# Kernel optimization log

Hardware: AMD Instinct MI355X
Metric: run time of the kernel (lower is better)

Reference implementation:

```python
import jax, jax.numpy as jnp
import numpy as np

B, T, N, D = 16, 64, 22, 64
K, E, DT, H = 4, 8, 5, 64
KL_WEIGHT = 0.01


def setup_inputs() -> dict:
    key = jax.random.key(0)
    ks = jax.random.split(key, 4)
    x = jax.random.normal(ks[0], (B, T, N, D), jnp.float32)
    # fixed-degree neighbor table: joint j's neighbors are (j..j+3) mod N, self first
    nb = jnp.asarray((np.arange(N)[:, None] + np.arange(K)[None, :]) % N, jnp.int32)
    Fin = DT * K * D  # 1280 flattened local window feature
    W1 = jax.random.normal(ks[1], (N, E, Fin, H), jnp.float32) / np.float32(np.sqrt(Fin))
    b1 = jnp.zeros((N, E, H), jnp.float32)
    W2 = jax.random.normal(ks[2], (N, E, H, H), jnp.float32) / np.float32(np.sqrt(H))
    b2 = jnp.zeros((N, E, H), jnp.float32)
    W3 = jax.random.normal(ks[3], (N, E, H, D), jnp.float32) / np.float32(np.sqrt(H))
    b3 = jnp.zeros((N, E, D), jnp.float32)
    return {"x": x, "nb": nb, "W1": W1, "b1": b1, "W2": W2, "b2": b2, "W3": W3, "b3": b3}


def reference(x, nb, W1, b1, W2, b2, W3, b3):
    Bx, Tx, Nx, Dx = x.shape
    dt_half = DT // 2
    # all valid centers t in range(dt_half, T - dt_half - 1), batched (no python loop over t, j)
    ts = jnp.arange(dt_half, Tx - dt_half - 1)            # [Tw]
    offs = jnp.arange(-dt_half, dt_half + 1)              # [DT]
    win = x[:, ts[:, None] + offs[None, :]]               # [B,Tw,DT,N,D]
    dx = win[:, :, :, nb, :]                              # [B,Tw,DT,N,K,D] neighbor gather
    Tw = ts.shape[0]
    f = dx.transpose(0, 1, 3, 2, 4, 5).reshape(Bx, Tw, Nx, DT * K * Dx)  # [B,Tw,N,Fin]
    # per-joint per-expert MLP, fully batched
    h = jax.nn.relu(jnp.einsum('btnf,nefh->btneh', f, W1) + b1)
    h = jax.nn.relu(jnp.einsum('btneh,nehg->btneg', h, W2) + b2)
    pred = jnp.einsum('btneh,nehd->btned', h, W3) + b3    # [B,Tw,N,E,D]
    y = x[:, ts]                                          # [B,Tw,N,D] center-frame target
    err = jnp.mean((pred - y[:, :, :, None, :]) ** 2, axis=-1)  # [B,Tw,N,E]
    min_err = jnp.min(err, axis=-1)                       # winner-take-all (monopoly)
    expert_idx_all = jnp.argmin(err, axis=-1)             # [B,Tw,N]
    p = jax.nn.softmax(-err, axis=-1)
    kl = jnp.sum(p * (jnp.log(p + 1e-9) + jnp.log(jnp.float32(E))), axis=-1)  # KL to uniform
    per_tj = jnp.mean(min_err + KL_WEIGHT * kl, axis=0)   # [Tw,N] batch-mean local losses
    # original divides by the FINAL loop indices j and t (off-by-one kept for fidelity)
    total = jnp.sum(per_tj) / jnp.float32(Nx - 1) / jnp.float32(Tx - dt_half - 2)
    expert_idx = expert_idx_all[:, -1, -1]                # last (t, j) iteration, [B]
    return total, expert_idx
```

## Files before the change

kernel.cpp:

```cpp
#include <hip/hip_runtime.h>
#include <math.h>

#define B_   16
#define T_   64
#define N_   22
#define D_   64
#define K_   4
#define E_   8
#define H_   64
#define TW   59
#define M_   (B_ * TW)
#define NE_  (N_ * E_)
#define NDXT (N_ * D_)
#define XTOT (B_ * T_ * N_ * D_)

typedef __attribute__((ext_vector_type(8))) short short8;
typedef __attribute__((ext_vector_type(4))) float float4v;

union Frag {
    short8 s8;
    unsigned u[4];
};

#define ERRWS_BYTES  ((size_t)(M_ * N_ * E_) * 4)
#define XH_OFF       (ERRWS_BYTES)
#define XIMG_BYTES   ((size_t)XTOT * 2)
#define XL_OFF       (XH_OFF + XIMG_BYTES)

#define HIMG_ROW 68

__device__ inline void split2(float f, unsigned& hi, unsigned& lo) {
    unsigned u  = __float_as_uint(f);
    unsigned ht = u & 0xffff0000u;
    float rem   = f - __uint_as_float(ht);
    hi = u >> 16;
    lo = __float_as_uint(rem) >> 16;
}

__global__ __launch_bounds__(256) void xsplit_kernel(
    const float* __restrict__ x, short* __restrict__ xh, short* __restrict__ xl)
{
    int i = (blockIdx.x * 256 + threadIdx.x) * 4;
    if (i >= XTOT) return;
    float4 v = *(const float4*)(x + i);
    unsigned h0, h1, h2, h3, l0, l1, l2, l3;
    split2(v.x, h0, l0); split2(v.y, h1, l1);
    split2(v.z, h2, l2); split2(v.w, h3, l3);
    uint2 hp, lp;
    hp.x = h0 | (h1 << 16); hp.y = h2 | (h3 << 16);
    lp.x = l0 | (l1 << 16); lp.y = l2 | (l3 << 16);
    *(uint2*)(xh + i) = hp;
    *(uint2*)(xl + i) = lp;
}

__global__ __launch_bounds__(256, 3) void moe_err_kernel(
    const float* __restrict__ x, const short* __restrict__ xh,
    const short* __restrict__ xl, const int* __restrict__ nb,
    const float* __restrict__ W1, const float* __restrict__ W2,
    const float* __restrict__ W3,
    const float* __restrict__ b1, const float* __restrict__ b2,
    const float* __restrict__ b3, float* __restrict__ err_ws)
{
    const int tid = threadIdx.x;
    const int w   = tid >> 6;
    const int L   = tid & 63;
    const int g   = blockIdx.x;
    const int e   = g & 7;
    const int mt  = (g >> 3) & 7;
    const int n   = g >> 6;
    const int ne  = n * E_ + e;

    __shared__ __align__(16) char smem[51200];
    unsigned char* wbuf = (unsigned char*)smem;
    unsigned* himg = (unsigned*)(smem + 16384);

    const int lrow = L & 15;
    const int dseg = (L >> 4) * 8;
    const int ccol = L & 15;
    const int qrow = (L >> 4) * 4;
    const int rowbase = mt * 128 + w * 32;

    const short* xhrow[2];
    const short* xlrow[2];
    #pragma unroll
    for (int rt = 0; rt < 2; ++rt) {
        int m  = rowbase + rt * 16 + lrow;
        int mc = m < M_ ? m : M_ - 1;
        int b = mc / TW, t = mc % TW;
        size_t base = (size_t)(b * T_ + t) * NDXT;
        xhrow[rt] = xh + base;
        xlrow[rt] = xl + base;
    }

    const int o0 = __builtin_amdgcn_readfirstlane(nb[n * K_ + 0]) * D_;
    const int o1 = __builtin_amdgcn_readfirstlane(nb[n * K_ + 1]) * D_;
    const int o2 = __builtin_amdgcn_readfirstlane(nb[n * K_ + 2]) * D_;
    const int o3 = __builtin_amdgcn_readfirstlane(nb[n * K_ + 3]) * D_;

    const float* W1ne = W1 + (size_t)ne * (1280 * 64);
    const float* W2ne = W2 + (size_t)ne * 4096;
    const float* W3ne = W3 + (size_t)ne * 4096;

    float wf[2][8];
    uint4 wph[2], wpl[2];
    auto loadWf = [&](const float* src) {
        #pragma unroll
        for (int p = 0; p < 2; ++p) {
            const int pi = 2 * w + p;
            const float* sp = src + ((pi >> 2) * 32 + (L >> 4) * 8) * 64
                                  + ((pi & 3) * 16 + (L & 15));
            #pragma unroll
            for (int j = 0; j < 8; ++j) wf[p][j] = sp[j * 64];
        }
    };
    auto packW = [&]() {
        #pragma unroll
        for (int p = 0; p < 2; ++p) {
            unsigned hs[8], ls[8];
            #pragma unroll
            for (int j = 0; j < 8; ++j) split2(wf[p][j], hs[j], ls[j]);
            wph[p].x = hs[0] | (hs[1] << 16); wph[p].y = hs[2] | (hs[3] << 16);
            wph[p].z = hs[4] | (hs[5] << 16); wph[p].w = hs[6] | (hs[7] << 16);
            wpl[p].x = ls[0] | (ls[1] << 16); wpl[p].y = ls[2] | (ls[3] << 16);
            wpl[p].z = ls[4] | (ls[5] << 16); wpl[p].w = ls[6] | (ls[7] << 16);
        }
    };
    auto storeW = [&]() {
        #pragma unroll
        for (int p = 0; p < 2; ++p) {
            char* bp = (char*)wbuf + (size_t)(2 * w + p) * 2048 + (size_t)L * 16;
            *(uint4*)bp          = wph[p];
            *(uint4*)(bp + 1024) = wpl[p];
        }
    };
    auto bfrag = [&](int s2, int cf, int hl) -> short8 {
        return *(const short8*)(wbuf + (size_t)((s2 * 4 + cf) * 2 + hl) * 1024
                                     + (size_t)L * 16);
    };

    loadWf(W1ne);
    packW();

    float4v acc1[2][4];
    #pragma unroll
    for (int rt = 0; rt < 2; ++rt)
        #pragma unroll
        for (int cf = 0; cf < 4; ++cf) acc1[rt][cf] = (float4v)0.f;

    for (int dt = 0; dt < 5; ++dt) {
        #pragma unroll
        for (int kk = 0; kk < 4; ++kk) {
            const int c = dt * 4 + kk;
            __syncthreads();
            storeW();
            __syncthreads();

            const float* nsrc = (c < 19) ? (W1ne + (size_t)(c + 1) * 4096) : W2ne;
            loadWf(nsrc);

            const int okk = (kk == 0) ? o0 : ((kk == 1) ? o1 : ((kk == 2) ? o2 : o3));
            const int off = dt * NDXT + okk;

            Frag ah[2][2], al[2][2];
            #pragma unroll
            for (int s2 = 0; s2 < 2; ++s2)
                #pragma unroll
                for (int rt = 0; rt < 2; ++rt) {
                    ah[s2][rt].s8 = *(const short8*)(xhrow[rt] + off + s2 * 32 + dseg);
                    al[s2][rt].s8 = *(const short8*)(xlrow[rt] + off + s2 * 32 + dseg);
                }
            #pragma unroll
            for (int s2 = 0; s2 < 2; ++s2)
                #pragma unroll
                for (int cf = 0; cf < 4; ++cf) {
                    short8 bh = bfrag(s2, cf, 0);
                    short8 bl = bfrag(s2, cf, 1);
                    #pragma unroll
                    for (int rt = 0; rt < 2; ++rt) {
                        acc1[rt][cf] = __builtin_amdgcn_mfma_f32_16x16x32_bf16(ah[s2][rt].s8, bh, acc1[rt][cf], 0, 0, 0);
                        acc1[rt][cf] = __builtin_amdgcn_mfma_f32_16x16x32_bf16(ah[s2][rt].s8, bl, acc1[rt][cf], 0, 0, 0);
                        acc1[rt][cf] = __builtin_amdgcn_mfma_f32_16x16x32_bf16(al[s2][rt].s8, bh, acc1[rt][cf], 0, 0, 0);
                    }
                }
            packW();
        }
    }

    __syncthreads();
    storeW();
    loadWf(W3ne);
    #pragma unroll
    for (int cf = 0; cf < 4; ++cf) {
        float bv = b1[(size_t)ne * H_ + cf * 16 + ccol];
        #pragma unroll
        for (int rt = 0; rt < 2; ++rt)
            #pragma unroll
            for (int reg = 0; reg < 4; ++reg) {
                float hv = fmaxf(acc1[rt][cf][reg] + bv, 0.f);
                unsigned u  = __float_as_uint(hv);
                unsigned ht = u & 0xffff0000u;
                float rem   = hv - __uint_as_float(ht);
                himg[(w * 32 + rt * 16 + qrow + reg) * HIMG_ROW + cf * 16 + ccol] =
                    ht | (__float_as_uint(rem) >> 16);
            }
    }
    packW();
    __syncthreads();

    float4v acc2[2][4];
    #pragma unroll
    for (int rt = 0; rt < 2; ++rt)
        #pragma unroll
        for (int cf = 0; cf < 4; ++cf) acc2[rt][cf] = (float4v)0.f;
    #pragma unroll
    for (int s2 = 0; s2 < 2; ++s2) {
        Frag ah[2], al[2];
        #pragma unroll
        for (int rt = 0; rt < 2; ++rt) {
            const unsigned* hp = himg + (w * 32 + rt * 16 + lrow) * HIMG_ROW + s2 * 32 + dseg;
            uint4 u0 = *(const uint4*)hp;
            uint4 u1 = *(const uint4*)(hp + 4);
            unsigned uu[8] = {u0.x, u0.y, u0.z, u0.w, u1.x, u1.y, u1.z, u1.w};
            #pragma unroll
            for (int i = 0; i < 4; ++i) {
                ah[rt].u[i] = (uu[2 * i] >> 16) | (uu[2 * i + 1] & 0xffff0000u);
                al[rt].u[i] = (uu[2 * i] & 0xffffu) | (uu[2 * i + 1] << 16);
            }
        }
        #pragma unroll
        for (int cf = 0; cf < 4; ++cf) {
            short8 bh = bfrag(s2, cf, 0);
            short8 bl = bfrag(s2, cf, 1);
            #pragma unroll
            for (int rt = 0; rt < 2; ++rt) {
                acc2[rt][cf] = __builtin_amdgcn_mfma_f32_16x16x32_bf16(ah[rt].s8, bh, acc2[rt][cf], 0, 0, 0);
                acc2[rt][cf] = __builtin_amdgcn_mfma_f32_16x16x32_bf16(ah[rt].s8, bl, acc2[rt][cf], 0, 0, 0);
                acc2[rt][cf] = __builtin_amdgcn_mfma_f32_16x16x32_bf16(al[rt].s8, bh, acc2[rt][cf], 0, 0, 0);
            }
        }
    }

    __syncthreads();
    storeW();
    #pragma unroll
    for (int cf = 0; cf < 4; ++cf) {
        float bv = b2[(size_t)ne * H_ + cf * 16 + ccol];
        #pragma unroll
        for (int rt = 0; rt < 2; ++rt)
            #pragma unroll
            for (int reg = 0; reg < 4; ++reg) {
                float hv = fmaxf(acc2[rt][cf][reg] + bv, 0.f);
                unsigned u  = __float_as_uint(hv);
                unsigned ht = u & 0xffff0000u;
                float rem   = hv - __uint_as_float(ht);
                himg[(w * 32 + rt * 16 + qrow + reg) * HIMG_ROW + cf * 16 + ccol] =
                    ht | (__float_as_uint(rem) >> 16);
            }
    }
    __syncthreads();

    float4v acc3[2][4];
    #pragma unroll
    for (int rt = 0; rt < 2; ++rt)
        #pragma unroll
        for (int cf = 0; cf < 4; ++cf) acc3[rt][cf] = (float4v)0.f;
    #pragma unroll
    for (int s2 = 0; s2 < 2; ++s2) {
        Frag ah[2], al[2];
        #pragma unroll
        for (int rt = 0; rt < 2; ++rt) {
            const unsigned* hp = himg + (w * 32 + rt * 16 + lrow) * HIMG_ROW + s2 * 32 + dseg;
            uint4 u0 = *(const uint4*)hp;
            uint4 u1 = *(const uint4*)(hp + 4);
            unsigned uu[8] = {u0.x, u0.y, u0.z, u0.w, u1.x, u1.y, u1.z, u1.w};
            #pragma unroll
            for (int i = 0; i < 4; ++i) {
                ah[rt].u[i] = (uu[2 * i] >> 16) | (uu[2 * i + 1] & 0xffff0000u);
                al[rt].u[i] = (uu[2 * i] & 0xffffu) | (uu[2 * i + 1] << 16);
            }
        }
        #pragma unroll
        for (int cf = 0; cf < 4; ++cf) {
            short8 bh = bfrag(s2, cf, 0);
            short8 bl = bfrag(s2, cf, 1);
            #pragma unroll
            for (int rt = 0; rt < 2; ++rt) {
                acc3[rt][cf] = __builtin_amdgcn_mfma_f32_16x16x32_bf16(ah[rt].s8, bh, acc3[rt][cf], 0, 0, 0);
                acc3[rt][cf] = __builtin_amdgcn_mfma_f32_16x16x32_bf16(ah[rt].s8, bl, acc3[rt][cf], 0, 0, 0);
                acc3[rt][cf] = __builtin_amdgcn_mfma_f32_16x16x32_bf16(al[rt].s8, bh, acc3[rt][cf], 0, 0, 0);
            }
        }
    }

    {
        float b3v[4];
        #pragma unroll
        for (int cf = 0; cf < 4; ++cf) b3v[cf] = b3[(size_t)ne * D_ + cf * 16 + ccol];

        #pragma unroll
        for (int rt = 0; rt < 2; ++rt) {
            #pragma unroll
            for (int reg = 0; reg < 4; ++reg) {
                const int m  = rowbase + rt * 16 + qrow + reg;
                const int mc = m < M_ ? m : M_ - 1;
                const int b = mc / TW, t = mc % TW;
                const float* yp = x + ((size_t)(b * T_ + t + 2) * N_ + n) * D_;
                float s = 0.f;
                #pragma unroll
                for (int cf = 0; cf < 4; ++cf) {
                    float d = acc3[rt][cf][reg] + b3v[cf] - yp[cf * 16 + ccol];
                    s += d * d;
                }
                s += __shfl_xor(s, 1);
                s += __shfl_xor(s, 2);
                s += __shfl_xor(s, 4);
                s += __shfl_xor(s, 8);
                if (ccol == 0 && m < M_) {
                    err_ws[((size_t)m * N_ + n) * E_ + e] = s * (1.f / 64.f);
                }
            }
        }
    }
}

__global__ __launch_bounds__(256) void moe_reduce_kernel(
    const float* __restrict__ err_ws, float* __restrict__ out)
{
    const int tid = threadIdx.x;
    const int idx = blockIdx.x * 256 + tid;
    float v = 0.f;
    if (idx < M_ * N_) {
        const int m = idx / N_, n = idx % N_;
        const float* ep = err_ws + (size_t)idx * E_;
        float ev[E_];
        float mn = ep[0];
        int am = 0;
        ev[0] = mn;
        #pragma unroll
        for (int i = 1; i < E_; ++i) {
            ev[i] = ep[i];
            if (ev[i] < mn) { mn = ev[i]; am = i; }
        }
        float p[E_];
        float Z = 0.f;
        #pragma unroll
        for (int i = 0; i < E_; ++i) { p[i] = expf(mn - ev[i]); Z += p[i]; }
        const float invZ = 1.f / Z;
        float kl = 0.f;
        #pragma unroll
        for (int i = 0; i < E_; ++i) {
            float q = p[i] * invZ;
            kl += q * (logf(q + 1e-9f) + 2.0794415416798357f);
        }
        v = mn + 0.01f * kl;
        const int t = m % TW, b = m / TW;
        if (t == TW - 1 && n == N_ - 1) out[1 + b] = (float)am;
    }
    __shared__ float sd[256];
    sd[tid] = v;
    __syncthreads();
    for (int s = 128; s > 0; s >>= 1) {
        if (tid < s) sd[tid] += sd[tid + s];
        __syncthreads();
    }
    if (tid == 0) atomicAdd(out, sd[0] * (1.f / 20160.f));
}

__global__ void init_out_kernel(float* out)
{
    if (threadIdx.x == 0) out[0] = 0.f;
}

extern "C" void kernel_launch(void* const* d_in, const int* in_sizes, int n_in,
                              void* d_out, int out_size, void* d_ws, size_t ws_size,
                              hipStream_t stream)
{
    const float* x  = (const float*)d_in[0];
    const int*   nb = (const int*)d_in[1];
    const float* W1 = (const float*)d_in[2];
    const float* b1 = (const float*)d_in[3];
    const float* W2 = (const float*)d_in[4];
    const float* b2 = (const float*)d_in[5];
    const float* W3 = (const float*)d_in[6];
    const float* b3 = (const float*)d_in[7];
    float* out    = (float*)d_out;
    float* err_ws = (float*)d_ws;
    short* xh     = (short*)((char*)d_ws + XH_OFF);
    short* xl     = (short*)((char*)d_ws + XL_OFF);

    hipLaunchKernelGGL(init_out_kernel, dim3(1), dim3(64), 0, stream, out);
    hipLaunchKernelGGL(xsplit_kernel, dim3(1408), dim3(256), 0, stream, x, xh, xl);
    hipLaunchKernelGGL(moe_err_kernel, dim3(NE_ * 8), dim3(256), 0, stream,
                       x, xh, xl, nb, W1, W2, W3, b1, b2, b3, err_ws);
    const int nred = (M_ * N_ + 255) / 256;
    hipLaunchKernelGGL(moe_reduce_kernel, dim3(nred), dim3(256), 0, stream, err_ws, out);
}
```

Before: 254.9 us.

## Double-buffer weight prefetch, reorder block mapping, single-block reduce without init kernel

Weight chunks for the first layer are now prefetched two stages ahead into a double-buffered register set, which hides global load latency behind the MFMA work. Blocks are remapped so consecutive block ids share the same expert and differ by row tile, which improves L2 reuse of the expert's weights. The reduction becomes one 1024-thread block that loops over all rows, uses vectorised loads and writes the total directly, so the init kernel and the atomic are no longer needed. In exchange the double buffer raises register pressure, which can hurt occupancy at 3 waves per SIMD, and the single-block reduce serialises that stage.

```diff
diff --git a/kernel.cpp b/kernel.cpp
--- a/kernel.cpp
+++ b/kernel.cpp
@@ -65,8 +65,8 @@
     const int w   = tid >> 6;
     const int L   = tid & 63;
     const int g   = blockIdx.x;
-    const int e   = g & 7;
-    const int mt  = (g >> 3) & 7;
+    const int mt  = g & 7;
+    const int e   = (g >> 3) & 7;
     const int n   = g >> 6;
     const int ne  = n * E_ + e;
 
@@ -100,25 +100,28 @@
     const float* W1ne = W1 + (size_t)ne * (1280 * 64);
     const float* W2ne = W2 + (size_t)ne * 4096;
     const float* W3ne = W3 + (size_t)ne * 4096;
-
-    float wf[2][8];
+    auto csrc = [&](int c) {
+        return c < 20 ? (W1ne + (size_t)c * 4096) : (c == 20 ? W2ne : W3ne);
+    };
+
+    float wf[2][2][8];
     uint4 wph[2], wpl[2];
-    auto loadWf = [&](const float* src) {
+    auto loadWf = [&](int wb, const float* src) {
         #pragma unroll
         for (int p = 0; p < 2; ++p) {
             const int pi = 2 * w + p;
             const float* sp = src + ((pi >> 2) * 32 + (L >> 4) * 8) * 64
                                   + ((pi & 3) * 16 + (L & 15));
             #pragma unroll
-            for (int j = 0; j < 8; ++j) wf[p][j] = sp[j * 64];
-        }
-    };
-    auto packW = [&]() {
+            for (int j = 0; j < 8; ++j) wf[wb][p][j] = sp[j * 64];
+        }
+    };
+    auto packW = [&](int wb) {
         #pragma unroll
         for (int p = 0; p < 2; ++p) {
             unsigned hs[8], ls[8];
             #pragma unroll
-            for (int j = 0; j < 8; ++j) split2(wf[p][j], hs[j], ls[j]);
+            for (int j = 0; j < 8; ++j) split2(wf[wb][p][j], hs[j], ls[j]);
             wph[p].x = hs[0] | (hs[1] << 16); wph[p].y = hs[2] | (hs[3] << 16);
             wph[p].z = hs[4] | (hs[5] << 16); wph[p].w = hs[6] | (hs[7] << 16);
             wpl[p].x = ls[0] | (ls[1] << 16); wpl[p].y = ls[2] | (ls[3] << 16);
@@ -138,8 +141,9 @@
                                      + (size_t)L * 16);
     };
 
-    loadWf(W1ne);
-    packW();
+    loadWf(0, csrc(0));
+    loadWf(1, csrc(1));
+    packW(0);
 
     float4v acc1[2][4];
     #pragma unroll
@@ -155,8 +159,7 @@
             storeW();
             __syncthreads();
 
-            const float* nsrc = (c < 19) ? (W1ne + (size_t)(c + 1) * 4096) : W2ne;
-            loadWf(nsrc);
+            loadWf(c & 1, csrc(c + 2 <= 21 ? c + 2 : 21));
 
             const int okk = (kk == 0) ? o0 : ((kk == 1) ? o1 : ((kk == 2) ? o2 : o3));
             const int off = dt * NDXT + okk;
@@ -182,13 +185,12 @@
                         acc1[rt][cf] = __builtin_amdgcn_mfma_f32_16x16x32_bf16(al[s2][rt].s8, bh, acc1[rt][cf], 0, 0, 0);
                     }
                 }
-            packW();
+            packW((c + 1) & 1);
         }
     }
 
     __syncthreads();
     storeW();
-    loadWf(W3ne);
     #pragma unroll
     for (int cf = 0; cf < 4; ++cf) {
         float bv = b1[(size_t)ne * H_ + cf * 16 + ccol];
@@ -204,7 +206,7 @@
                     ht | (__float_as_uint(rem) >> 16);
             }
     }
-    packW();
+    packW(1);
     __syncthreads();
 
     float4v acc2[2][4];
@@ -323,22 +325,23 @@
     }
 }
 
-__global__ __launch_bounds__(256) void moe_reduce_kernel(
+__global__ __launch_bounds__(1024) void moe_reduce_kernel(
     const float* __restrict__ err_ws, float* __restrict__ out)
 {
     const int tid = threadIdx.x;
-    const int idx = blockIdx.x * 256 + tid;
-    float v = 0.f;
-    if (idx < M_ * N_) {
+    float partial = 0.f;
+    for (int idx = tid; idx < M_ * N_; idx += 1024) {
         const int m = idx / N_, n = idx % N_;
         const float* ep = err_ws + (size_t)idx * E_;
         float ev[E_];
-        float mn = ep[0];
+        float4 e0 = *(const float4*)ep;
+        float4 e1 = *(const float4*)(ep + 4);
+        ev[0] = e0.x; ev[1] = e0.y; ev[2] = e0.z; ev[3] = e0.w;
+        ev[4] = e1.x; ev[5] = e1.y; ev[6] = e1.z; ev[7] = e1.w;
+        float mn = ev[0];
         int am = 0;
-        ev[0] = mn;
         #pragma unroll
         for (int i = 1; i < E_; ++i) {
-            ev[i] = ep[i];
             if (ev[i] < mn) { mn = ev[i]; am = i; }
         }
         float p[E_];
@@ -352,23 +355,18 @@
             float q = p[i] * invZ;
             kl += q * (logf(q + 1e-9f) + 2.0794415416798357f);
         }
-        v = mn + 0.01f * kl;
+        partial += mn + 0.01f * kl;
         const int t = m % TW, b = m / TW;
         if (t == TW - 1 && n == N_ - 1) out[1 + b] = (float)am;
     }
-    __shared__ float sd[256];
-    sd[tid] = v;
-    __syncthreads();
-    for (int s = 128; s > 0; s >>= 1) {
+    __shared__ float sd[1024];
+    sd[tid] = partial;
+    __syncthreads();
+    for (int s = 512; s > 0; s >>= 1) {
         if (tid < s) sd[tid] += sd[tid + s];
         __syncthreads();
     }
-    if (tid == 0) atomicAdd(out, sd[0] * (1.f / 20160.f));
-}
-
-__global__ void init_out_kernel(float* out)
-{
-    if (threadIdx.x == 0) out[0] = 0.f;
+    if (tid == 0) out[0] = sd[0] * (1.f / 20160.f);
 }
 
 extern "C" void kernel_launch(void* const* d_in, const int* in_sizes, int n_in,
@@ -388,10 +386,8 @@
     short* xh     = (short*)((char*)d_ws + XH_OFF);
     short* xl     = (short*)((char*)d_ws + XL_OFF);
 
-    hipLaunchKernelGGL(init_out_kernel, dim3(1), dim3(64), 0, stream, out);
     hipLaunchKernelGGL(xsplit_kernel, dim3(1408), dim3(256), 0, stream, x, xh, xl);
     hipLaunchKernelGGL(moe_err_kernel, dim3(NE_ * 8), dim3(256), 0, stream,
                        x, xh, xl, nb, W1, W2, W3, b1, b2, b3, err_ws);
-    const int nred = (M_ * N_ + 255) / 256;
-    hipLaunchKernelGGL(moe_reduce_kernel, dim3(nred), dim3(256), 0, stream, err_ws, out);
-}
+    hipLaunchKernelGGL(moe_reduce_kernel, dim3(1), dim3(1024), 0, stream, err_ws, out);
+}
```

Measured after the change: 282.3 us. 1.11x slower.
